# Optimization experiments

Hardware: AMD Instinct MI355X
Metric: run time of the kernel (lower is better)

Reference implementation:

```python
import jax, jax.numpy as jnp
import numpy as np

LN_EPS = 1e-5
IH_IDX = np.array([0, 2, 4, 6])  # layernorm_iih, fih, aih, oih
HH_IDX = np.array([1, 3, 5, 7])  # layernorm_ihh, fhh, ahh, ohh


def _ln(x, g, b):
    # LayerNorm over last dim, matching nn.LayerNorm(hidden_size)
    mu = jnp.mean(x, axis=-1, keepdims=True)
    xc = x - mu
    var = jnp.mean(xc * xc, axis=-1, keepdims=True)
    return g * xc * jax.lax.rsqrt(var + LN_EPS) + b


def setup_inputs() -> dict:
    B, I, H = 4096, 1024, 1024
    key = jax.random.key(0)
    ks = jax.random.split(key, 8)
    stdv = 1.0 / np.sqrt(H)  # reset_parameters: uniform(-stdv, stdv)
    return {
        "x": jax.random.normal(ks[0], (B, I), jnp.float32),
        "h": jax.random.normal(ks[1], (B, H), jnp.float32),
        "c": jax.random.normal(ks[2], (B, H), jnp.float32),
        "w_ih": jax.random.uniform(ks[3], (4 * H, I), jnp.float32, -stdv, stdv),
        "w_hh": jax.random.uniform(ks[4], (4 * H, H), jnp.float32, -stdv, stdv),
        "b_ih": jax.random.uniform(ks[5], (4 * H,), jnp.float32, -stdv, stdv),
        # 9 LayerNorms stacked: [iih, ihh, fih, fhh, aih, ahh, oih, ohh, ct]
        "ln_gamma": 1.0 + 0.1 * jax.random.normal(ks[6], (9, H), jnp.float32),
        "ln_beta": 0.1 * jax.random.normal(ks[7], (9, H), jnp.float32),
        "time": 0,
    }


def reference(x, h, c, w_ih, w_hh, b_ih, ln_gamma, ln_beta, time):
    B = x.shape[0]
    H = w_hh.shape[1]
    # pre-activations, split into the 4 gates (i, f, a, o) along dim 1
    pre_ih = (x @ w_ih.T).reshape(B, 4, H)   # [B,4,H]
    pre_hh = (h @ w_hh.T).reshape(B, 4, H)   # [B,4,H]
    # per-gate LayerNorm on ih and hh contributions, then add bias
    gates = (
        _ln(pre_ih, ln_gamma[IH_IDX], ln_beta[IH_IDX])
        + _ln(pre_hh, ln_gamma[HH_IDX], ln_beta[HH_IDX])
        + b_ih.reshape(4, H)
    )
    i, f, a, o = gates[:, 0], gates[:, 1], gates[:, 2], gates[:, 3]
    c_new = jax.nn.sigmoid(f) * c + jax.nn.sigmoid(i) * jnp.tanh(a)
    h_new = jax.nn.sigmoid(o) * jnp.tanh(_ln(c_new, ln_gamma[8], ln_beta[8]))
    return (h_new, c_new)
```

## Files before the change

### kernel.cpp

```cpp
#include <hip/hip_runtime.h>
#include <hip/hip_bf16.h>
#include <stdint.h>


#define HDIM 1024
#define BATCH 4096
#define NGATE 4096
#define KDIM 1024

typedef __bf16 bf16x8 __attribute__((ext_vector_type(8)));
typedef float f32x4 __attribute__((ext_vector_type(4)));
typedef unsigned short ushort8_t __attribute__((ext_vector_type(8)));

__device__ __forceinline__ unsigned short f2bf(float f) {
  unsigned int u = __builtin_bit_cast(unsigned int, f);
  unsigned int r = (u + 0x7fffu + ((u >> 16) & 1u)) >> 16;
  return (unsigned short)r;
}

__device__ __forceinline__ float bf2f(unsigned short s) {
  unsigned int u = ((unsigned int)s) << 16;
  return __builtin_bit_cast(float, u);
}

__device__ __forceinline__ void gl_lds16(const void* g, void* l) {
  __builtin_amdgcn_global_load_lds(
      (__attribute__((address_space(1))) unsigned int*)g,
      (__attribute__((address_space(3))) unsigned int*)l,
      16, 0, 0);
}

__global__ __launch_bounds__(256) void cast_bf16_kernel(
    const float* __restrict__ x, const float* __restrict__ h,
    const float* __restrict__ wi, const float* __restrict__ wh,
    unsigned short* __restrict__ xb, unsigned short* __restrict__ hb,
    unsigned short* __restrict__ wib, unsigned short* __restrict__ whb) {
  const float* src;
  unsigned short* dst;
  switch (blockIdx.y) {
    case 0: src = x;  dst = xb;  break;
    case 1: src = h;  dst = hb;  break;
    case 2: src = wi; dst = wib; break;
    default: src = wh; dst = whb; break;
  }
  size_t base = ((size_t)blockIdx.x * 256 + threadIdx.x) * 8;
  const size_t stride = (size_t)512 * 256 * 8;
#pragma unroll
  for (int it = 0; it < 4; ++it) {
    float4 v0 = *(const float4*)(src + base);
    float4 v1 = *(const float4*)(src + base + 4);
    ushort8_t o;
    o[0] = f2bf(v0.x); o[1] = f2bf(v0.y); o[2] = f2bf(v0.z); o[3] = f2bf(v0.w);
    o[4] = f2bf(v1.x); o[5] = f2bf(v1.y); o[6] = f2bf(v1.z); o[7] = f2bf(v1.w);
    *(ushort8_t*)(dst + base) = o;
    base += stride;
  }
}

__global__ __launch_bounds__(256, 4) void gemm_bt_kernel(
    const unsigned short* __restrict__ A0, const unsigned short* __restrict__ B0,
    unsigned short* __restrict__ C0,
    const unsigned short* __restrict__ A1, const unsigned short* __restrict__ B1,
    unsigned short* __restrict__ C1) {
  const unsigned short* A = blockIdx.z ? A1 : A0;
  const unsigned short* B = blockIdx.z ? B1 : B0;
  unsigned short* C = blockIdx.z ? C1 : C0;

  __shared__ alignas(16) unsigned short As[128 * 64];
  __shared__ alignas(16) unsigned short Bs[128 * 64];

  const int tid = threadIdx.x;
  const int wave = tid >> 6;
  const int lane = tid & 63;
  const int bm = blockIdx.x * 128;
  const int bn = blockIdx.y * 128;
  const int wm = (wave >> 1) * 64;
  const int wn = (wave & 1) * 64;

  const int srow = lane >> 3;
  const int scol = (((lane & 7) ^ (lane >> 3)) * 8);

  f32x4 acc[4][4];
#pragma unroll
  for (int i = 0; i < 4; ++i)
#pragma unroll
    for (int j = 0; j < 4; ++j)
#pragma unroll
      for (int r = 0; r < 4; ++r) acc[i][j][r] = 0.0f;

  const int m15 = lane & 15;
  const int quad = lane >> 4;

  for (int k0 = 0; k0 < KDIM; k0 += 64) {
#pragma unroll
    for (int t = 0; t < 4; ++t) {
      int R = wave * 32 + t * 8;
      gl_lds16(A + (size_t)(bm + R + srow) * KDIM + k0 + scol, &As[R * 64]);
      gl_lds16(B + (size_t)(bn + R + srow) * KDIM + k0 + scol, &Bs[R * 64]);
    }
    __syncthreads();

#pragma unroll
    for (int s = 0; s < 2; ++s) {
      bf16x8 af[4], bfr[4];
#pragma unroll
      for (int i = 0; i < 4; ++i) {
        int row = wm + i * 16 + m15;
        af[i] = *(const bf16x8*)&As[row * 64 + (((4 * s + quad) ^ (m15 & 7)) * 8)];
      }
#pragma unroll
      for (int j = 0; j < 4; ++j) {
        int row = wn + j * 16 + m15;
        bfr[j] = *(const bf16x8*)&Bs[row * 64 + (((4 * s + quad) ^ (m15 & 7)) * 8)];
      }
#pragma unroll
      for (int i = 0; i < 4; ++i)
#pragma unroll
        for (int j = 0; j < 4; ++j)
          acc[i][j] = __builtin_amdgcn_mfma_f32_16x16x32_bf16(af[i], bfr[j], acc[i][j], 0, 0, 0);
    }

    __syncthreads();
  }

#pragma unroll
  for (int i = 0; i < 4; ++i)
#pragma unroll
    for (int j = 0; j < 4; ++j)
#pragma unroll
      for (int r = 0; r < 4; ++r) {
        int m = bm + wm + i * 16 + quad * 4 + r;
        int n = bn + wn + j * 16 + m15;
        C[(size_t)m * NGATE + n] = f2bf(acc[i][j][r]);
      }
}

__device__ __forceinline__ float fast_sigmoid(float x) {
  return __builtin_amdgcn_rcpf(1.0f + __expf(-x));
}
__device__ __forceinline__ float fast_tanh(float x) {
  return 1.0f - 2.0f * __builtin_amdgcn_rcpf(__expf(2.0f * x) + 1.0f);
}

__global__ __launch_bounds__(256) void ln_gate_kernel(
    const unsigned short* __restrict__ pih, const unsigned short* __restrict__ phh,
    const float* __restrict__ c, const float* __restrict__ b_ih,
    const float* __restrict__ gamma, const float* __restrict__ beta,
    float* __restrict__ h_out, float* __restrict__ c_out) {
  __shared__ float gbuf[4][1024];
  __shared__ float red[8];
  const int b = blockIdx.x;
  const int t = threadIdx.x;
  const int g = t >> 6;
  const int lane = t & 63;
  const float inv_h = 1.0f / 1024.0f;
  const float eps = 1e-5f;

  {
    const size_t rb = (size_t)b * NGATE + g * HDIM;
    float vih[16], vhh[16];
    float s0 = 0.f, q0 = 0.f, s1 = 0.f, q1 = 0.f;
#pragma unroll
    for (int s = 0; s < 4; ++s) {
      const int hh = lane * 4 + s * 256;
      ushort4 a4 = *(const ushort4*)&pih[rb + hh];
      ushort4 e4 = *(const ushort4*)&phh[rb + hh];
      vih[s * 4 + 0] = bf2f(a4.x); vih[s * 4 + 1] = bf2f(a4.y);
      vih[s * 4 + 2] = bf2f(a4.z); vih[s * 4 + 3] = bf2f(a4.w);
      vhh[s * 4 + 0] = bf2f(e4.x); vhh[s * 4 + 1] = bf2f(e4.y);
      vhh[s * 4 + 2] = bf2f(e4.z); vhh[s * 4 + 3] = bf2f(e4.w);
#pragma unroll
      for (int r = 0; r < 4; ++r) {
        float va = vih[s * 4 + r], ea = vhh[s * 4 + r];
        s0 += va; q0 += va * va;
        s1 += ea; q1 += ea * ea;
      }
    }
#pragma unroll
    for (int o = 1; o < 64; o <<= 1) {
      s0 += __shfl_xor(s0, o, 64); q0 += __shfl_xor(q0, o, 64);
      s1 += __shfl_xor(s1, o, 64); q1 += __shfl_xor(q1, o, 64);
    }
    const float mu0 = s0 * inv_h;
    const float rs0 = rsqrtf(q0 * inv_h - mu0 * mu0 + eps);
    const float mu1 = s1 * inv_h;
    const float rs1 = rsqrtf(q1 * inv_h - mu1 * mu1 + eps);

#pragma unroll
    for (int s = 0; s < 4; ++s) {
      const int hh = lane * 4 + s * 256;
      float4 g0 = *(const float4*)&gamma[(2 * g) * HDIM + hh];
      float4 b0 = *(const float4*)&beta[(2 * g) * HDIM + hh];
      float4 g1 = *(const float4*)&gamma[(2 * g + 1) * HDIM + hh];
      float4 b1 = *(const float4*)&beta[(2 * g + 1) * HDIM + hh];
      float4 bb = *(const float4*)&b_ih[g * HDIM + hh];
      const float* g0p = &g0.x; const float* b0p = &b0.x;
      const float* g1p = &g1.x; const float* b1p = &b1.x;
      const float* bbp = &bb.x;
      float4 out;
      float* op = &out.x;
#pragma unroll
      for (int r = 0; r < 4; ++r) {
        float gih = g0p[r] * ((vih[s * 4 + r] - mu0) * rs0) + b0p[r];
        float ghh = g1p[r] * ((vhh[s * 4 + r] - mu1) * rs1) + b1p[r];
        op[r] = gih + ghh + bbp[r];
      }
      *(float4*)&gbuf[g][hh] = out;
    }
  }
  __syncthreads();

  const int j = t * 4;
  float4 iv4 = *(const float4*)&gbuf[0][j];
  float4 fv4 = *(const float4*)&gbuf[1][j];
  float4 av4 = *(const float4*)&gbuf[2][j];
  float4 ov4 = *(const float4*)&gbuf[3][j];
  const float* ivp = &iv4.x; const float* fvp = &fv4.x;
  const float* avp = &av4.x; const float* ovp = &ov4.x;

  float4 cv4 = *(const float4*)&c[(size_t)b * HDIM + j];
  const float* cvp = &cv4.x;
  float cn[4], ov[4];
  float s2 = 0.f, q2 = 0.f;
#pragma unroll
  for (int r = 0; r < 4; ++r) {
    float iv = fast_sigmoid(ivp[r]);
    float fv = fast_sigmoid(fvp[r]);
    float av = fast_tanh(avp[r]);
    ov[r] = fast_sigmoid(ovp[r]);
    float cvn = fv * cvp[r] + iv * av;
    cn[r] = cvn;
    s2 += cvn; q2 += cvn * cvn;
  }
#pragma unroll
  for (int o = 1; o < 64; o <<= 1) {
    s2 += __shfl_xor(s2, o, 64);
    q2 += __shfl_xor(q2, o, 64);
  }
  if (lane == 0) { red[g * 2] = s2; red[g * 2 + 1] = q2; }
  __syncthreads();
  s2 = red[0] + red[2] + red[4] + red[6];
  q2 = red[1] + red[3] + red[5] + red[7];
  float mu = s2 * inv_h;
  float rs = rsqrtf(q2 * inv_h - mu * mu + eps);

  float4 g8 = *(const float4*)&gamma[8 * HDIM + j];
  float4 b8 = *(const float4*)&beta[8 * HDIM + j];
  const float* g8p = &g8.x; const float* b8p = &b8.x;
  float4 ho, co;
  float* hop = &ho.x; float* cop = &co.x;
#pragma unroll
  for (int r = 0; r < 4; ++r) {
    float ln = g8p[r] * ((cn[r] - mu) * rs) + b8p[r];
    hop[r] = ov[r] * fast_tanh(ln);
    cop[r] = cn[r];
  }
  *(float4*)&h_out[(size_t)b * HDIM + j] = ho;
  *(float4*)&c_out[(size_t)b * HDIM + j] = co;
}

extern "C" void kernel_launch(void* const* d_in, const int* in_sizes, int n_in,
                              void* d_out, int out_size, void* d_ws, size_t ws_size,
                              hipStream_t stream) {
  const float* x     = (const float*)d_in[0];
  const float* h     = (const float*)d_in[1];
  const float* c     = (const float*)d_in[2];
  const float* w_ih  = (const float*)d_in[3];
  const float* w_hh  = (const float*)d_in[4];
  const float* b_ih  = (const float*)d_in[5];
  const float* gamma = (const float*)d_in[6];
  const float* beta  = (const float*)d_in[7];

  char* ws = (char*)d_ws;
  unsigned short* xb  = (unsigned short*)(ws);
  unsigned short* hb  = (unsigned short*)(ws + (size_t)8 * 1024 * 1024);
  unsigned short* wib = (unsigned short*)(ws + (size_t)16 * 1024 * 1024);
  unsigned short* whb = (unsigned short*)(ws + (size_t)24 * 1024 * 1024);
  unsigned short* pih = (unsigned short*)(ws + (size_t)32 * 1024 * 1024);
  unsigned short* phh = (unsigned short*)(ws + (size_t)64 * 1024 * 1024);

  dim3 cgrid(512, 4, 1);
  cast_bf16_kernel<<<cgrid, 256, 0, stream>>>(x, h, w_ih, w_hh, xb, hb, wib, whb);

  dim3 ggrid(32, 32, 2);
  gemm_bt_kernel<<<ggrid, 256, 0, stream>>>(xb, wib, pih, hb, whb, phh);

  float* h_out = (float*)d_out;
  float* c_out = h_out + (size_t)BATCH * HDIM;
  ln_gate_kernel<<<4096, 256, 0, stream>>>(pih, phh, c, b_ih, gamma, beta, h_out, c_out);
}
```

Measured before the change: 232.9 us.

## Rewrite GEMM as 256x256 tile, 8-wave kernel with multi-buffered LDS pipeline

The bf16 GEMM moves from 128x128 tiles with 4 waves and single-buffered LDS to 256x256 tiles with 8 waves. It uses a four-slot LDS ring where global-to-LDS loads for later k-steps are issued while MFMAs run on the current ones, coordinated by explicit barriers, waitcnt and setprio. Block indices are swizzled so consecutive blocks are spread across the tile grid, which may improve L2 locality. The aim is to hide memory latency and raise data reuse per LDS load, at the cost of more registers, a larger LDS footprint and fewer blocks per CU.

```diff
diff --git a/kernel.cpp b/kernel.cpp
--- a/kernel.cpp
+++ b/kernel.cpp
@@ -29,6 +29,11 @@
       (__attribute__((address_space(3))) unsigned int*)l,
       16, 0, 0);
 }
+
+#define BAR() asm volatile("s_barrier" ::: "memory")
+#define WAITL() asm volatile("s_waitcnt lgkmcnt(0)" ::: "memory")
+#define WAITV(N) asm volatile("s_waitcnt vmcnt(" #N ")" ::: "memory")
+#define SCHED0() __builtin_amdgcn_sched_barrier(0)
 
 __global__ __launch_bounds__(256) void cast_bf16_kernel(
     const float* __restrict__ x, const float* __restrict__ h,
@@ -57,82 +62,166 @@
   }
 }
 
-__global__ __launch_bounds__(256, 4) void gemm_bt_kernel(
-    const unsigned short* __restrict__ A0, const unsigned short* __restrict__ B0,
-    unsigned short* __restrict__ C0,
-    const unsigned short* __restrict__ A1, const unsigned short* __restrict__ B1,
-    unsigned short* __restrict__ C1) {
-  const unsigned short* A = blockIdx.z ? A1 : A0;
-  const unsigned short* B = blockIdx.z ? B1 : B0;
-  unsigned short* C = blockIdx.z ? C1 : C0;
-
-  __shared__ alignas(16) unsigned short As[128 * 64];
-  __shared__ alignas(16) unsigned short Bs[128 * 64];
+__global__ __launch_bounds__(512, 2) void gemm_bt_kernel(
+    const unsigned short* __restrict__ A0p, const unsigned short* __restrict__ B0p,
+    unsigned short* __restrict__ C0p,
+    const unsigned short* __restrict__ A1p, const unsigned short* __restrict__ B1p,
+    unsigned short* __restrict__ C1p) {
+  const int flat = blockIdx.x + (blockIdx.y << 4) + (blockIdx.z << 8);
+  const int swz = ((flat & 7) << 6) | (flat >> 3);
+  const int bz = swz >> 8;
+  const unsigned short* A = bz ? A1p : A0p;
+  const unsigned short* B = bz ? B1p : B0p;
+  unsigned short* C = bz ? C1p : C0p;
+  const int bm = (swz & 15) * 256;
+  const int bn = ((swz >> 4) & 15) * 256;
+
+  __shared__ alignas(16) unsigned short As[4 * 8192];
+  __shared__ alignas(16) unsigned short Bs[4 * 8192];
 
   const int tid = threadIdx.x;
   const int wave = tid >> 6;
   const int lane = tid & 63;
-  const int bm = blockIdx.x * 128;
-  const int bn = blockIdx.y * 128;
-  const int wm = (wave >> 1) * 64;
-  const int wn = (wave & 1) * 64;
+  const int wr = wave >> 2;
+  const int wc = wave & 3;
 
   const int srow = lane >> 3;
-  const int scol = (((lane & 7) ^ (lane >> 3)) * 8);
-
-  f32x4 acc[4][4];
-#pragma unroll
-  for (int i = 0; i < 4; ++i)
-#pragma unroll
-    for (int j = 0; j < 4; ++j)
-#pragma unroll
-      for (int r = 0; r < 4; ++r) acc[i][j][r] = 0.0f;
-
+  const int scol = ((lane & 7) ^ (lane >> 3)) * 8;
   const int m15 = lane & 15;
   const int quad = lane >> 4;
-
-  for (int k0 = 0; k0 < KDIM; k0 += 64) {
-#pragma unroll
-    for (int t = 0; t < 4; ++t) {
-      int R = wave * 32 + t * 8;
-      gl_lds16(A + (size_t)(bm + R + srow) * KDIM + k0 + scol, &As[R * 64]);
-      gl_lds16(B + (size_t)(bn + R + srow) * KDIM + k0 + scol, &Bs[R * 64]);
-    }
-    __syncthreads();
-
-#pragma unroll
-    for (int s = 0; s < 2; ++s) {
-      bf16x8 af[4], bfr[4];
-#pragma unroll
-      for (int i = 0; i < 4; ++i) {
-        int row = wm + i * 16 + m15;
-        af[i] = *(const bf16x8*)&As[row * 64 + (((4 * s + quad) ^ (m15 & 7)) * 8)];
-      }
-#pragma unroll
-      for (int j = 0; j < 4; ++j) {
-        int row = wn + j * 16 + m15;
-        bfr[j] = *(const bf16x8*)&Bs[row * 64 + (((4 * s + quad) ^ (m15 & 7)) * 8)];
-      }
-#pragma unroll
-      for (int i = 0; i < 4; ++i)
-#pragma unroll
-        for (int j = 0; j < 4; ++j)
-          acc[i][j] = __builtin_amdgcn_mfma_f32_16x16x32_bf16(af[i], bfr[j], acc[i][j], 0, 0, 0);
-    }
-
-    __syncthreads();
-  }
-
-#pragma unroll
-  for (int i = 0; i < 4; ++i)
+  const int sw = m15 & 7;
+
+  const unsigned short* gwA = A + (size_t)(bm + wave * 8 + srow) * KDIM + scol;
+  const unsigned short* gwB = B + (size_t)(bn + wave * 8 + srow) * KDIM + scol;
+
+  f32x4 acc[8][4];
+#pragma unroll
+  for (int i = 0; i < 8; ++i)
 #pragma unroll
     for (int j = 0; j < 4; ++j)
 #pragma unroll
-      for (int r = 0; r < 4; ++r) {
-        int m = bm + wm + i * 16 + quad * 4 + r;
-        int n = bn + wn + j * 16 + m15;
-        C[(size_t)m * NGATE + n] = f2bf(acc[i][j][r]);
-      }
+      for (int r = 0; r < 4; ++r) acc[i][j][r] = 0.0f;
+
+  auto stage = [&](const unsigned short* gw, int goff, int kk, unsigned short* slot) {
+    gl_lds16(gw + (size_t)goff * KDIM + kk, slot + wave * 512);
+    gl_lds16(gw + (size_t)(goff + 64) * KDIM + kk, slot + wave * 512 + 4096);
+  };
+
+  bf16x8 af[4][2], b0[2][2], b1[2][2];
+
+  auto ldA = [&](const unsigned short* base) {
+#pragma unroll
+    for (int i2 = 0; i2 < 4; ++i2) {
+      int r = wr * 64 + i2 * 16 + m15;
+#pragma unroll
+      for (int s = 0; s < 2; ++s)
+        af[i2][s] = *(const bf16x8*)&base[r * 64 + (((s * 4 + quad) ^ sw) << 3)];
+    }
+  };
+  auto ldB = [&](const unsigned short* base, bf16x8 (&bf)[2][2]) {
+#pragma unroll
+    for (int j2 = 0; j2 < 2; ++j2) {
+      int r = wc * 32 + j2 * 16 + m15;
+#pragma unroll
+      for (int s = 0; s < 2; ++s)
+        bf[j2][s] = *(const bf16x8*)&base[r * 64 + (((s * 4 + quad) ^ sw) << 3)];
+    }
+  };
+
+#define MMA16(H, G, BF)                                                       \
+  do {                                                                        \
+    __builtin_amdgcn_s_setprio(1);                                            \
+    _Pragma("unroll") for (int i2 = 0; i2 < 4; ++i2)                          \
+        _Pragma("unroll") for (int j2 = 0; j2 < 2; ++j2) {                    \
+      acc[(H)*4 + i2][(G)*2 + j2] = __builtin_amdgcn_mfma_f32_16x16x32_bf16(  \
+          af[i2][0], BF[j2][0], acc[(H)*4 + i2][(G)*2 + j2], 0, 0, 0);        \
+      acc[(H)*4 + i2][(G)*2 + j2] = __builtin_amdgcn_mfma_f32_16x16x32_bf16(  \
+          af[i2][1], BF[j2][1], acc[(H)*4 + i2][(G)*2 + j2], 0, 0, 0);        \
+    }                                                                         \
+    __builtin_amdgcn_s_setprio(0);                                            \
+  } while (0)
+
+  stage(gwA, 0,   0,  &As[0]);
+  stage(gwB, 0,   0,  &Bs[0]);
+  stage(gwB, 128, 0,  &Bs[1 * 8192]);
+  stage(gwA, 128, 0,  &As[1 * 8192]);
+  stage(gwA, 0,   64, &As[2 * 8192]);
+  stage(gwB, 0,   64, &Bs[2 * 8192]);
+  stage(gwB, 128, 64, &Bs[3 * 8192]);
+  WAITV(6);
+  BAR();
+
+  for (int u = 0; u < 8; ++u) {
+    const int kO1 = ((2 * u + 1) & 15) * 64;
+    const int kE2 = ((2 * u + 2) & 15) * 64;
+    const int kO2 = ((2 * u + 3) & 15) * 64;
+
+    ldA(&As[0]);
+    ldB(&Bs[0], b0);
+    stage(gwA, 128, kO1, &As[3 * 8192]);
+    BAR(); WAITL(); SCHED0();
+    MMA16(0, 0, b0);
+    BAR();
+
+    ldB(&Bs[1 * 8192], b1);
+    stage(gwA, 0, kE2, &As[0]);
+    BAR(); WAITL(); SCHED0();
+    MMA16(0, 1, b1);
+    WAITV(8);
+    BAR();
+
+    ldA(&As[1 * 8192]);
+    stage(gwB, 0, kE2, &Bs[0]);
+    BAR(); WAITL(); SCHED0();
+    MMA16(1, 1, b1);
+    BAR();
+
+    stage(gwB, 128, kE2, &Bs[1 * 8192]);
+    BAR();
+    MMA16(1, 0, b0);
+    WAITV(8);
+    BAR();
+
+    ldA(&As[2 * 8192]);
+    ldB(&Bs[2 * 8192], b0);
+    stage(gwA, 128, kE2, &As[1 * 8192]);
+    BAR(); WAITL(); SCHED0();
+    MMA16(0, 0, b0);
+    BAR();
+
+    ldB(&Bs[3 * 8192], b1);
+    stage(gwA, 0, kO2, &As[2 * 8192]);
+    BAR(); WAITL(); SCHED0();
+    MMA16(0, 1, b1);
+    WAITV(8);
+    BAR();
+
+    ldA(&As[3 * 8192]);
+    stage(gwB, 0, kO2, &Bs[2 * 8192]);
+    BAR(); WAITL(); SCHED0();
+    MMA16(1, 1, b1);
+    BAR();
+
+    stage(gwB, 128, kO2, &Bs[3 * 8192]);
+    BAR();
+    MMA16(1, 0, b0);
+    WAITV(8);
+    BAR();
+  }
+  WAITV(0);
+
+#pragma unroll
+  for (int i = 0; i < 8; ++i) {
+    int m = bm + (i >> 2) * 128 + wr * 64 + (i & 3) * 16 + quad * 4;
+#pragma unroll
+    for (int j = 0; j < 4; ++j) {
+      int n = bn + (j >> 1) * 128 + wc * 32 + (j & 1) * 16 + m15;
+#pragma unroll
+      for (int rr = 0; rr < 4; ++rr)
+        C[(size_t)(m + rr) * NGATE + n] = f2bf(acc[i][j][rr]);
+    }
+  }
+#undef MMA16
 }
 
 __device__ __forceinline__ float fast_sigmoid(float x) {
@@ -282,8 +371,8 @@
   dim3 cgrid(512, 4, 1);
   cast_bf16_kernel<<<cgrid, 256, 0, stream>>>(x, h, w_ih, w_hh, xb, hb, wib, whb);
 
-  dim3 ggrid(32, 32, 2);
-  gemm_bt_kernel<<<ggrid, 256, 0, stream>>>(xb, wib, pih, hb, whb, phh);
+  dim3 ggrid(16, 16, 2);
+  gemm_bt_kernel<<<ggrid, 512, 0, stream>>>(xb, wib, pih, hb, whb, phh);
 
   float* h_out = (float*)d_out;
   float* c_out = h_out + (size_t)BATCH * HDIM;
```

Result: no change. 233.9 us (+0.4%).
